# Kernel tuning notes

Measured on AMD Instinct MI355X. Metric: run time of the kernel, lower is better.

The kernel has to match this reference:

```python
import jax, jax.numpy as jnp
import numpy as np

B, LQ, LD = 64, 20, 512
D, NB, WIN = 300, 11, 5
EQ, ED, DESC, KC = 5, 10, 20, 10
VW, VE, VC = 50000, 10000, 5000

# KNRM kernel centers / widths (requires_grad=False buffers in the original)
MU = jnp.array([1.0, 0.9, 0.7, 0.5, 0.3, 0.1, -0.1, -0.3, -0.5, -0.7, -0.9], jnp.float32)
SIGMA = jnp.array([1e-3] + [0.1] * 10, jnp.float32)


def setup_inputs() -> dict:
    key = jax.random.key(0)
    ks = jax.random.split(key, 20)
    f = lambda k, s, sc: jax.random.normal(k, s, jnp.float32) * sc
    return {
        "inputs_qwt": jax.random.randint(ks[0], (B, LQ), 0, VW),
        "inputs_qwm": jnp.ones((B, LQ), jnp.float32),
        "inputs_qei": jax.random.randint(ks[1], (B, EQ), 0, VE),
        "inputs_qet": jax.random.randint(ks[2], (B, EQ * DESC), 0, VW),
        "inputs_qew": jax.random.randint(ks[3], (B, EQ * KC), 0, VC),
        "inputs_qem": jnp.ones((B, EQ), jnp.float32),
        "inputs_dwt": jax.random.randint(ks[4], (B, LD), 0, VW),
        "inputs_dwm": jnp.ones((B, LD), jnp.float32),
        "inputs_dei": jax.random.randint(ks[5], (B, ED), 0, VE),
        "inputs_det": jax.random.randint(ks[6], (B, ED * DESC), 0, VW),
        "inputs_dew": jax.random.randint(ks[7], (B, ED * KC), 0, VC),
        "inputs_dem": jnp.ones((B, ED), jnp.float32),
        "wrd_emb": f(ks[8], (VW, D), 0.1),
        "ent_emb": f(ks[9], (VE, 128), 0.1),
        "car_emb": f(ks[10], (VC, 128), 0.1),
        "bow_W": f(ks[11], (128, D), 0.05), "bow_b": jnp.zeros((128,), jnp.float32),
        "conv_uni_W": f(ks[12], (128, 1, D), 0.05), "conv_uni_b": jnp.zeros((128,), jnp.float32),
        "conv_bi_W": f(ks[13], (128, 2, D), 0.04), "conv_bi_b": jnp.zeros((128,), jnp.float32),
        "conv_tri_W": f(ks[14], (128, 3, D), 0.03), "conv_tri_b": jnp.zeros((128,), jnp.float32),
        "conv_des_W": f(ks[15], (128, WIN, D), 0.02), "conv_des_b": jnp.zeros((128,), jnp.float32),
        "dense_f_W": f(ks[16], (1, 16 * NB), 0.1), "dense_f_b": jnp.zeros((1,), jnp.float32),
    }


def _conv_words(x, w, b):
    # x: [N, L, D]; w: [O, k, D] -> relu conv over the word axis, valid padding -> [N, L-k+1, O]
    k, L = w.shape[1], x.shape[1]
    segs = jnp.stack([x[:, i:L - k + 1 + i] for i in range(k)], axis=2)  # [N, L-k+1, k, D]
    return jax.nn.relu(jnp.einsum('nlkd,okd->nlo', segs, w) + b)


def _l2(x):
    return x / jnp.maximum(jnp.linalg.norm(x, axis=-1, keepdims=True), 1e-10)


def _kernel_pool(q, d, mq, md):
    # q:[B,Lq,128] d:[B,Ld,128] mq:[B,Lq] md:[B,Ld] -> [B, NB]
    sim = jnp.einsum('bqe,bde->bqd', q, d)
    pv = jnp.exp(-0.5 * (sim[..., None] - MU) ** 2 / (SIGMA ** 2)) * md[:, None, :, None]
    lps = jnp.log(jnp.maximum(pv.sum(2), 1e-10)) * 0.01 * mq[:, :, None]
    return lps.sum(1)


def _forward(inputs_qwt, inputs_qwm, inputs_qei, inputs_qet, inputs_qew, inputs_qem,
             inputs_dwt, inputs_dwm, inputs_dei, inputs_det, inputs_dew, inputs_dem,
             wrd_emb, ent_emb, car_emb, bow_W, bow_b,
             conv_uni_W, conv_uni_b, conv_bi_W, conv_bi_b, conv_tri_W, conv_tri_b,
             conv_des_W, conv_des_b, dense_f_W, dense_f_b):
    b = inputs_qwt.shape[0]
    qw = wrd_emb[inputs_qwt]  # [B, LQ, D]
    dw = wrd_emb[inputs_dwt]  # [B, LD, D]

    def ent_branch(ids_e, ids_desc, ids_car, n_ent, w_bow):
        desc = wrd_emb[ids_desc].reshape(b * n_ent, DESC, D)
        e_conv = _conv_words(desc, conv_des_W, conv_des_b).max(1).reshape(b, n_ent, 128)
        t = car_emb[ids_car].reshape(b, n_ent * KC, 128)
        att = jax.nn.softmax((w_bow * t).sum(2).reshape(b, n_ent, KC, 1), axis=2)
        ew = (att * t.reshape(b, n_ent, KC, 128)).sum(2)
        return ent_emb[ids_e] + e_conv + ew

    qw_bow = (jnp.einsum('bld,od->blo', qw, bow_W) + bow_b).sum(1, keepdims=True)  # [B,1,128]
    dw_bow = (jnp.einsum('bld,od->blo', dw, bow_W) + bow_b).sum(1, keepdims=True)
    qs = _l2(ent_branch(inputs_qei, inputs_qet, inputs_qew, EQ, qw_bow))  # [B,5,128]
    ds = _l2(ent_branch(inputs_dei, inputs_det, inputs_dew, ED, dw_bow))  # [B,10,128]

    qu = _l2(_conv_words(qw, conv_uni_W, conv_uni_b))
    qb = _l2(_conv_words(qw, conv_bi_W, conv_bi_b))
    qt = _l2(_conv_words(qw, conv_tri_W, conv_tri_b))
    du = _l2(_conv_words(dw, conv_uni_W, conv_uni_b))
    db = _l2(_conv_words(dw, conv_bi_W, conv_bi_b))
    dt = _l2(_conv_words(dw, conv_tri_W, conv_tri_b))

    mqu, mqb, mqt = inputs_qwm, inputs_qwm[:, :-1], inputs_qwm[:, :-2]
    mdu, mdb, mdt = inputs_dwm, inputs_dwm[:, :-1], inputs_dwm[:, :-2]

    kp = _kernel_pool
    pools = [kp(qu, du, mqu, mdu), kp(qu, dt, mqu, mdt), kp(qu, db, mqu, mdb),
             kp(qb, du, mqb, mdu), kp(qt, du, mqt, mdu), kp(qb, db, mqb, mdb),
             kp(qb, dt, mqb, mdt), kp(qt, db, mqt, mdb), kp(qt, dt, mqt, mdt),
             kp(qs, du, inputs_qem, mdu), kp(qs, db, inputs_qem, mdb), kp(qs, dt, inputs_qem, mdt),
             kp(qu, ds, mqu, inputs_dem), kp(qb, ds, mqb, inputs_dem), kp(qt, ds, mqt, inputs_dem),
             kp(qs, ds, inputs_qem, inputs_dem)]
    feats = jnp.concatenate(pools, axis=1)  # [B, 16*NB]
    return jnp.tanh(feats @ dense_f_W.T + dense_f_b)[:, 0]


def reference(inputs_qwt, inputs_qwm, inputs_qei, inputs_qet, inputs_qew, inputs_qem,
              inputs_dwt, inputs_dwm, inputs_dei, inputs_det, inputs_dew, inputs_dem,
              wrd_emb, ent_emb, car_emb, bow_W, bow_b,
              conv_uni_W, conv_uni_b, conv_bi_W, conv_bi_b, conv_tri_W, conv_tri_b,
              conv_des_W, conv_des_b, dense_f_W, dense_f_b):
    return _forward(inputs_qwt, inputs_qwm, inputs_qei, inputs_qet, inputs_qew, inputs_qem,
                    inputs_dwt, inputs_dwm, inputs_dei, inputs_det, inputs_dew, inputs_dem,
                    wrd_emb, ent_emb, car_emb, bow_W, bow_b,
                    conv_uni_W, conv_uni_b, conv_bi_W, conv_bi_b, conv_tri_W, conv_tri_b,
                    conv_des_W, conv_des_b, dense_f_W, dense_f_b)
```

## Files before the change

kernel.cpp:

```cpp
#include <hip/hip_runtime.h>

typedef unsigned short u16;
typedef unsigned int u32;
typedef __attribute__((ext_vector_type(8))) short bf16x8;
typedef __attribute__((ext_vector_type(4))) float f32x4;

#define DEVI __device__ __forceinline__

namespace {
constexpr int LQ_ = 20, LD_ = 512, D_ = 300;
constexpr int EQ_ = 5, ED_ = 10, KC_ = 10;
constexpr int QROWS = 62, DROWS = 1543;
constexpr int QSTR = 64, DSTR = 1600;
constexpr float MU_H[11] = {1.0f,0.9f,0.7f,0.5f,0.3f,0.1f,-0.1f,-0.3f,-0.5f,-0.7f,-0.9f};
}

__constant__ int P2QT_C[16] = {0,0,0,1,2,1,1,2,2,3,3,3,0,1,2,3};
__constant__ int P2DT_C[16] = {0,2,1,0,0,1,2,1,2,0,1,2,3,3,3,3};
__constant__ int NP_C[4]   = {2,2,4,4};
__constant__ int PPL_C[16] = {0,1,0,0, 2,3,0,0, 2,3,4,5, 4,5,6,7};
__constant__ int SETL_C[16]= {0,0,0,0, 0,0,0,0, 1,1,0,0, 1,1,0,0};

DEVI u16 f2bf(float f){ union{float f;u32 u;} v; v.f=f; u32 r=(v.u+0x7fffu+((v.u>>16)&1u))>>16; return (u16)r; }
DEVI float bf2f(u16 h){ union{u32 u;float f;} v; v.u=((u32)h)<<16; return v.f; }

__global__ __launch_bounds__(256) void k_wpack(const float* __restrict__ Wu, const float* __restrict__ Wb,
                                               const float* __restrict__ Wt, const float* __restrict__ Wd,
                                               u16* __restrict__ Wp){
  const int ts = blockIdx.x/10, ks = blockIdx.x%10;
  const float* W; int kk, tap;
  if(ts==0){W=Wu;kk=1;tap=0;}
  else if(ts<3){W=Wb;kk=2;tap=ts-1;}
  else if(ts<6){W=Wt;kk=3;tap=ts-3;}
  else {W=Wd;kk=5;tap=ts-6;}
  for(int idx=threadIdx.x; idx<4096; idx+=256){
    int n0=idx>>9, lane=(idx>>3)&63, j=idx&7;
    int col=lane&15, kg=lane>>4;
    int d=ks*32+kg*8+j, o=n0*16+col;
    float v = (d<300)? W[((long)o*kk + tap)*300 + d] : 0.f;
    Wp[(((long)(ts*8+n0)*10+ks)*64 + lane)*8 + j] = f2bf(v);
  }
}

__global__ __launch_bounds__(512) void k_main(
    const int* __restrict__ dwt, const int* __restrict__ qwt,
    const int* __restrict__ qet, const int* __restrict__ det,
    const float* __restrict__ emb, const u16* __restrict__ Wp,
    const float* __restrict__ bu, const float* __restrict__ bb, const float* __restrict__ bt,
    const float* __restrict__ bd,
    u16* __restrict__ dcat, u16* __restrict__ qcat,
    float* __restrict__ qdm, float* __restrict__ ddm, float* __restrict__ parts)
{
  __shared__ __align__(16) char smem[77088];
  __shared__ int tokid[80];
  const int bx = blockIdx.x, t = threadIdx.x;
  const int lane=t&63, wave=t>>6, col16=lane&15, kg=lane>>4;
  if(bx < 576){
    const bool isdoc = bx < 512;
    const int seq   = isdoc? (bx>>3) : (bx-512);
    const int l0    = isdoc? (bx&7)*64 : 0;
    const int Ltok  = isdoc? LD_ : LQ_;
    u16* outp = isdoc? dcat : qcat;
    const long seqstride = isdoc? (long)DSTR*128 : (long)QSTR*128;
    u16* xs = (u16*)smem;
    float* ot = (float*)(smem + 43296);
    const int nrows = min(66, Ltok - l0);
    if(t<66) tokid[t] = (t<nrows)? (isdoc? dwt[seq*LD_+l0+t] : qwt[seq*LQ_+t]) : 0;
    __syncthreads();
    for(int idx=t; idx<66*80; idx+=512){
      int r=idx/80, q=idx-r*80;
      ushort4 o4;
      if(q<75 && r<nrows){
        float4 v = ((const float4*)(emb + (long)tokid[r]*D_))[q];
        o4.x=f2bf(v.x); o4.y=f2bf(v.y); o4.z=f2bf(v.z); o4.w=f2bf(v.w);
      } else { o4.x=0;o4.y=0;o4.z=0;o4.w=0; }
      *(ushort4*)&xs[r*328 + q*4] = o4;
    }
    __syncthreads();
    #pragma unroll
    for(int c=0;c<3;c++){
      const int tb = (c==0)?0:((c==1)?1:3);
      const int base = (c==0)?0:((c==1)?Ltok:2*Ltok-1);
      const float* bias = (c==0)?bu:((c==1)?bb:bt);
      f32x4 acc4[4];
      #pragma unroll
      for(int mt=0;mt<4;mt++) acc4[mt]=(f32x4){0.f,0.f,0.f,0.f};
      #pragma unroll
      for(int h=0;h<2;h++){
        bf16x8 wf[15];
        #pragma unroll
        for(int i=0;i<=c;i++)
          #pragma unroll
          for(int k5=0;k5<5;k5++)
            wf[i*5+k5] = *(const bf16x8*)(Wp + (((long)((tb+i)*8 + wave)*10) + h*5 + k5)*512 + lane*8);
        #pragma unroll
        for(int mt=0;mt<4;mt++){
          #pragma unroll
          for(int i=0;i<=c;i++){
            const u16* xrow = &xs[(mt*16 + col16 + i)*328 + h*160 + kg*8];
            #pragma unroll
            for(int k5=0;k5<5;k5++){
              bf16x8 a = *(const bf16x8*)(xrow + k5*32);
              acc4[mt]=__builtin_amdgcn_mfma_f32_16x16x32_bf16(a,wf[i*5+k5],acc4[mt],0,0,0);
            }
          }
        }
      }
      const float bv = bias[wave*16+col16];
      #pragma unroll
      for(int mt=0;mt<4;mt++)
        #pragma unroll
        for(int reg=0;reg<4;reg++)
          ot[(mt*16+kg*4+reg)*132 + wave*16+col16] = fmaxf(acc4[mt][reg]+bv, 0.f);
      __syncthreads();
      {
        const int p = t>>3, j = t&7;
        const int nv = min(64, (Ltok - c) - l0);
        float ss=0.f;
        if(p<nv){
          #pragma unroll
          for(int k=0;k<16;k++){ float v = ot[p*132 + j + 8*k]; ss += v*v; }
        }
        ss += __shfl_xor(ss,1); ss += __shfl_xor(ss,2); ss += __shfl_xor(ss,4);
        if(p<nv){
          float inv = 1.0f/fmaxf(sqrtf(ss),1e-10f);
          u16* ob = outp + (long)seq*seqstride + ((long)(base + l0 + p))*128 + j*16;
          #pragma unroll
          for(int hh=0;hh<2;hh++){
            bf16x8 o8;
            #pragma unroll
            for(int e=0;e<8;e++) o8[e] = (short)f2bf(ot[p*132 + j*16 + hh*8 + e]*inv);
            *(bf16x8*)(ob + hh*8) = o8;
          }
        }
      }
      __syncthreads();
    }
  } else if(bx < 816){
    const int d = bx - 576;
    const bool isq = d < 80;
    const int s0 = (isq? d : d-80)*4;
    const int* dt_ = isq? qet : det;
    float* dm = isq? qdm : ddm;
    u16* xs4 = (u16*)smem;
    if(t<80) tokid[t] = dt_[s0*20 + t];
    __syncthreads();
    for(int idx=t; idx<80*80; idx+=512){
      int lr=idx/80, q=idx-lr*80;
      ushort4 o4;
      if(q<75){
        float4 v = ((const float4*)(emb + (long)tokid[lr]*D_))[q];
        o4.x=f2bf(v.x); o4.y=f2bf(v.y); o4.z=f2bf(v.z); o4.w=f2bf(v.w);
      } else { o4.x=0;o4.y=0;o4.z=0;o4.w=0; }
      *(ushort4*)&xs4[lr*328 + q*4] = o4;
    }
    __syncthreads();
    f32x4 acc4[4];
    #pragma unroll
    for(int s=0;s<4;s++) acc4[s]=(f32x4){0.f,0.f,0.f,0.f};
    #pragma unroll
    for(int h=0;h<2;h++){
      bf16x8 wf[25];
      #pragma unroll
      for(int tap=0;tap<5;tap++)
        #pragma unroll
        for(int k5=0;k5<5;k5++)
          wf[tap*5+k5] = *(const bf16x8*)(Wp + (((long)((6+tap)*8 + wave)*10) + h*5 + k5)*512 + lane*8);
      #pragma unroll
      for(int s=0;s<4;s++){
        #pragma unroll
        for(int tap=0;tap<5;tap++){
          const u16* xrow = &xs4[(s*20 + col16 + tap)*328 + h*160 + kg*8];
          #pragma unroll
          for(int k5=0;k5<5;k5++){
            bf16x8 a = *(const bf16x8*)(xrow + k5*32);
            acc4[s]=__builtin_amdgcn_mfma_f32_16x16x32_bf16(a,wf[tap*5+k5],acc4[s],0,0,0);
          }
        }
      }
    }
    const float bv = bd[wave*16+col16];
    #pragma unroll
    for(int s=0;s<4;s++){
      float m=-1e30f;
      #pragma unroll
      for(int reg=0;reg<4;reg++) m=fmaxf(m, acc4[s][reg]+bv);
      m=fmaxf(m,__shfl_xor(m,16));
      m=fmaxf(m,__shfl_xor(m,32));
      m=fmaxf(m,0.f);
      if(kg==0) dm[(long)(s0+s)*128 + wave*16+col16]=m;
    }
  } else {
    const int idx = bx - 816;
    const int side = idx>>6, b = idx&63;
    const int q = t%80, g = t/80;
    if(g<6){
      float a0=0.f,a1=0.f,a2=0.f,a3=0.f;
      const int L = side? LD_ : LQ_;
      if(q<75){
        for(int r=g; r<L; r+=6){
          const int tok = side? dwt[b*LD_+r] : qwt[b*LQ_+r];
          float4 v = ((const float4*)(emb + (long)tok*D_))[q];
          a0+=v.x; a1+=v.y; a2+=v.z; a3+=v.w;
        }
      }
      if(q<76){
        float4 o4={a0,a1,a2,a3};
        *(float4*)(parts + (((long)side*64 + b)*8 + g)*304 + q*4) = o4;
      }
    }
  }
}

__global__ __launch_bounds__(256) void k_entpost(
    const int* __restrict__ qei, const int* __restrict__ qew,
    const int* __restrict__ dei, const int* __restrict__ dew,
    const float* __restrict__ qdm, const float* __restrict__ ddm,
    const float* __restrict__ parts, const float* __restrict__ bowW, const float* __restrict__ bowb,
    const float* __restrict__ ent, const float* __restrict__ car,
    u16* __restrict__ qcat, u16* __restrict__ dcat)
{
  const int e15 = blockIdx.x, b = blockIdx.y, t = threadIdx.x;
  const bool isq = (e15 < EQ_);
  const int e = isq? e15 : e15-EQ_;
  const float* dmx = isq? (qdm + (long)(b*EQ_+e)*128) : (ddm + (long)(b*ED_+e)*128);
  const int eid = isq? qei[b*EQ_+e] : dei[b*ED_+e];
  const int* carids = isq? (qew + b*EQ_*KC_ + e*KC_) : (dew + b*ED_*KC_ + e*KC_);
  u16* orow = isq? (qcat + ((long)b*QSTR + 57 + e)*128) : (dcat + ((long)b*DSTR + 1533 + e)*128);

  __shared__ float carS[KC_*128];
  __shared__ float sv[304];
  __shared__ float bwS[128];
  __shared__ float sc[KC_], att[KC_];
  __shared__ float red[4];
  const float* p = parts + (((long)(isq?0:1)*64 + b)*8)*304;
  for(int d=t; d<304; d+=256){
    float s=0.f;
    #pragma unroll
    for(int g=0;g<6;g++) s += p[g*304+d];
    sv[d]=s;
  }
  for(int idx=t; idx<KC_*128; idx+=256){
    int j = idx>>7, c = idx&127;
    carS[j*128+c] = car[(long)carids[j]*128 + c];
  }
  __syncthreads();
  {
    const int ch = t>>1, h = t&1;
    float acc=0.f;
    const float* w = bowW + (long)ch*300 + h*150;
    const float* x = sv + h*150;
    for(int d=0; d<150; d++) acc += x[d]*w[d];
    acc += __shfl_xor(acc,1);
    if(h==0) bwS[ch] = acc + (isq? (float)LQ_ : (float)LD_)*bowb[ch];
  }
  __syncthreads();
  {
    const int j = t>>4, l16 = t&15;
    if(j < KC_){
      float s=0.f;
      for(int c=l16;c<128;c+=16) s += bwS[c]*carS[j*128+c];
      s += __shfl_xor(s,1); s += __shfl_xor(s,2); s += __shfl_xor(s,4); s += __shfl_xor(s,8);
      if(l16==0) sc[j]=s;
    }
  }
  __syncthreads();
  if(t==0){
    float m=-1e30f;
    for(int x=0;x<KC_;x++) m = fmaxf(m, sc[x]);
    float ssum=0.f;
    for(int x=0;x<KC_;x++){ float e2=__expf(sc[x]-m); att[x]=e2; ssum+=e2; }
    float rs = 1.0f/ssum;
    for(int x=0;x<KC_;x++) att[x]*=rs;
  }
  __syncthreads();
  float val=0.f;
  if(t<128){
    float ew=0.f;
    for(int x=0;x<KC_;x++) ew += att[x]*carS[x*128+t];
    val = ent[(long)eid*128+t] + dmx[t] + ew;
  }
  float ss = val*val;
  ss += __shfl_xor(ss,1); ss += __shfl_xor(ss,2); ss += __shfl_xor(ss,4);
  ss += __shfl_xor(ss,8); ss += __shfl_xor(ss,16); ss += __shfl_xor(ss,32);
  if((t&63)==0) red[t>>6]=ss;
  __syncthreads();
  if(t<128){
    float nv = 1.0f/fmaxf(sqrtf(red[0]+red[1]),1e-10f);
    orow[t] = f2bf(val*nv);
  }
}

__global__ __launch_bounds__(512) void k_simgauss(const u16* __restrict__ qcat, const u16* __restrict__ dcat,
                                                  const float* __restrict__ dwm, const float* __restrict__ dem,
                                                  float* __restrict__ Spart){
  const int b=blockIdx.x, piece=blockIdx.y;
  const int t=threadIdx.x, lane=t&63, wave=t>>6;
  const int qtile=wave>>1, dpar=wave&1;
  const int col16=lane&15, kg=lane>>4;
  constexpr int NT[4]={8,8,8,1};
  constexpr int TBASE[4]={0,8,16,24};
  constexpr int PEND[4]={512,1023,1533,1543};
  bf16x8 afr[4];
  #pragma unroll
  for(int ks=0;ks<4;ks++)
    afr[ks] = *(const bf16x8*)&qcat[((long)b*QSTR + qtile*16+col16)*128 + ks*32 + kg*8];
  float aP[4][11], aS[4][11];
  #pragma unroll
  for(int r=0;r<4;r++)
    #pragma unroll
    for(int m=0;m<11;m++){ aP[r][m]=0.f; aS[r][m]=0.f; }
  const int t0 = dpar*4;
  const int t1 = (NT[piece] < t0+4)? NT[piece] : t0+4;
  for(int tt=t0; tt<t1; tt++){
    const int tb = TBASE[piece]+tt;
    f32x4 acc[4];
    #pragma unroll
    for(int n0=0;n0<4;n0++) acc[n0]=(f32x4){0.f,0.f,0.f,0.f};
    #pragma unroll
    for(int ks=0;ks<4;ks++){
      #pragma unroll
      for(int n0=0;n0<4;n0++){
        bf16x8 bfr = *(const bf16x8*)&dcat[((long)b*DSTR + tb*64 + n0*16+col16)*128 + ks*32 + kg*8];
        acc[n0]=__builtin_amdgcn_mfma_f32_16x16x32_bf16(afr[ks],bfr,acc[n0],0,0,0);
      }
    }
    #pragma unroll
    for(int n0=0;n0<4;n0++){
      const int col = tb*64 + n0*16 + col16;
      float md;
      if(col<512) md = dwm[b*LD_+col];
      else if(col<1023) md = dwm[b*LD_+col-512];
      else if(col<1533) md = dwm[b*LD_+col-1023];
      else if(col<1543) md = dem[b*ED_+(col-1533)];
      else md = 0.f;
      const bool pr = col < PEND[piece];
      const float mdP = pr? md : 0.f;
      const float mdS = pr? 0.f : md;
      #pragma unroll
      for(int reg=0;reg<4;reg++){
        const float svv = acc[n0][reg];
        {
          float d1 = svv-1.0f;
          float e = __expf(-500000.0f*d1*d1);
          aP[reg][0] += mdP*e; aS[reg][0] += mdS*e;
        }
        #pragma unroll
        for(int m=1;m<11;m++){
          float dm = svv-MU_H[m];
          float e = __expf(-50.0f*dm*dm);
          aP[reg][m] += mdP*e; aS[reg][m] += mdS*e;
        }
      }
    }
  }
  #pragma unroll
  for(int reg=0;reg<4;reg++)
    #pragma unroll
    for(int m=0;m<11;m++){
      float vP=aP[reg][m];
      vP+=__shfl_xor(vP,1); vP+=__shfl_xor(vP,2); vP+=__shfl_xor(vP,4); vP+=__shfl_xor(vP,8);
      aP[reg][m]=vP;
      float vS=aS[reg][m];
      vS+=__shfl_xor(vS,1); vS+=__shfl_xor(vS,2); vS+=__shfl_xor(vS,4); vS+=__shfl_xor(vS,8);
      aS[reg][m]=vS;
    }
  if(col16==0){
    #pragma unroll
    for(int reg=0;reg<4;reg++){
      const int qr = qtile*16 + kg*4 + reg;
      float* o = Spart + (((long)b*64 + qr)*8 + piece*2+dpar)*22;
      #pragma unroll
      for(int m=0;m<11;m++){ o[m]=aP[reg][m]; o[11+m]=aS[reg][m]; }
    }
  }
}

__global__ __launch_bounds__(256) void k_feats(const float* __restrict__ Spart, const float* __restrict__ qwm,
                                               const float* __restrict__ qem, const float* __restrict__ dfW,
                                               const float* __restrict__ dfb, float* __restrict__ out){
  const int b = blockIdx.x, t = threadIdx.x;
  __shared__ float fsh[176];
  __shared__ float red[4];
  if(t<176){
    const int pool = t/11, m = t - pool*11;
    const int qt = P2QT_C[pool], dt = P2DT_C[pool];
    const int qlo = (qt==0)?0:((qt==1)?20:((qt==2)?39:57));
    const int qn  = (qt==0)?20:((qt==1)?19:((qt==2)?18:5));
    float f = 0.f;
    for(int r=0;r<qn;r++){
      const int qr = qlo + r;
      float mq = (qt<3)? qwm[b*LQ_+r] : qem[b*EQ_+r];
      const float* row = Spart + (((long)b*64 + qr)*8)*22 + m;
      float sv = 0.f;
      const int np = NP_C[dt];
      for(int k=0;k<np;k++){
        const int ii = dt*4+k;
        sv += row[PPL_C[ii]*22 + SETL_C[ii]*11];
      }
      f += logf(fmaxf(sv,1e-10f))*0.01f*mq;
    }
    fsh[t] = f;
  }
  __syncthreads();
  float v = (t<176)? fsh[t]*dfW[t] : 0.f;
  v += __shfl_xor(v,1); v += __shfl_xor(v,2); v += __shfl_xor(v,4);
  v += __shfl_xor(v,8); v += __shfl_xor(v,16); v += __shfl_xor(v,32);
  if((t&63)==0) red[t>>6]=v;
  __syncthreads();
  if(t==0) out[b] = tanhf(red[0]+red[1]+red[2]+red[3] + dfb[0]);
}

extern "C" void kernel_launch(void* const* d_in, const int* in_sizes, int n_in,
                              void* d_out, int out_size, void* d_ws, size_t ws_size,
                              hipStream_t stream)
{
  const int*   qwt=(const int*)d_in[0];
  const float* qwm=(const float*)d_in[1];
  const int*   qei=(const int*)d_in[2];
  const int*   qet=(const int*)d_in[3];
  const int*   qew=(const int*)d_in[4];
  const float* qem=(const float*)d_in[5];
  const int*   dwt=(const int*)d_in[6];
  const float* dwm=(const float*)d_in[7];
  const int*   dei=(const int*)d_in[8];
  const int*   det=(const int*)d_in[9];
  const int*   dew=(const int*)d_in[10];
  const float* dem=(const float*)d_in[11];
  const float* emb=(const float*)d_in[12];
  const float* ent=(const float*)d_in[13];
  const float* car=(const float*)d_in[14];
  const float* bowW=(const float*)d_in[15];
  const float* bowb=(const float*)d_in[16];
  const float* Wu=(const float*)d_in[17];
  const float* bu=(const float*)d_in[18];
  const float* Wb=(const float*)d_in[19];
  const float* bb=(const float*)d_in[20];
  const float* Wt=(const float*)d_in[21];
  const float* bt=(const float*)d_in[22];
  const float* Wd=(const float*)d_in[23];
  const float* bd=(const float*)d_in[24];
  const float* dfW=(const float*)d_in[25];
  const float* dfb=(const float*)d_in[26];
  float* out=(float*)d_out;

  char* ws=(char*)d_ws;
  size_t off=0;
  auto A=[&](size_t n){ size_t r=off; off=(off+n+255)&~(size_t)255; return r; };
  u16* Wp     = (u16*)(ws + A((size_t)11*8*10*64*8*2));
  u16* dcat   = (u16*)(ws + A((size_t)64*DSTR*128*2));
  u16* qcat   = (u16*)(ws + A((size_t)64*QSTR*128*2));
  float* qdm  = (float*)(ws + A((size_t)320*128*4));
  float* ddm  = (float*)(ws + A((size_t)640*128*4));
  float* parts= (float*)(ws + A((size_t)2*64*8*304*4));
  float* Spart= (float*)(ws + A((size_t)64*64*8*22*4));
  if(off > ws_size) return;

  k_wpack<<<110,256,0,stream>>>(Wu,Wb,Wt,Wd,Wp);
  k_main<<<944,512,0,stream>>>(dwt,qwt,qet,det,emb,Wp,bu,bb,bt,bd,dcat,qcat,qdm,ddm,parts);
  k_entpost<<<dim3(15,64),256,0,stream>>>(qei,qew,dei,dew,qdm,ddm,parts,bowW,bowb,ent,car,qcat,dcat);
  k_simgauss<<<dim3(64,4),512,0,stream>>>(qcat,dcat,dwm,dem,Spart);
  k_feats<<<64,256,0,stream>>>(Spart,qwm,qem,dfW,dfb,out);
}
```

Measured before the change: 179.6 us.

## Pre-convert embedding table to bf16 and fuse bag-of-words sums into main kernel

A new prep kernel converts the whole fp32 word-embedding table to bf16 on every call, alongside the weight packing. The main kernel's row gathers then read half-width bf16 rows. The separate bag-of-words gather blocks are removed: per-tile sums are now taken from the bf16 rows already staged in shared memory. A small new kernel does the bow projection instead of k_entpost. This targets the duplicated fp32 row gathers, but converting the full 50000-row table each call adds a large streaming pass, and the bow sums now accumulate bf16-rounded values.

```diff
diff --git a/kernel.cpp b/kernel.cpp
--- a/kernel.cpp
+++ b/kernel.cpp
@@ -12,6 +12,7 @@
 constexpr int EQ_ = 5, ED_ = 10, KC_ = 10;
 constexpr int QROWS = 62, DROWS = 1543;
 constexpr int QSTR = 64, DSTR = 1600;
+constexpr int NCVT = 14649;
 constexpr float MU_H[11] = {1.0f,0.9f,0.7f,0.5f,0.3f,0.1f,-0.1f,-0.3f,-0.5f,-0.7f,-0.9f};
 }
 
@@ -24,28 +25,40 @@
 DEVI u16 f2bf(float f){ union{float f;u32 u;} v; v.f=f; u32 r=(v.u+0x7fffu+((v.u>>16)&1u))>>16; return (u16)r; }
 DEVI float bf2f(u16 h){ union{u32 u;float f;} v; v.u=((u32)h)<<16; return v.f; }
 
-__global__ __launch_bounds__(256) void k_wpack(const float* __restrict__ Wu, const float* __restrict__ Wb,
-                                               const float* __restrict__ Wt, const float* __restrict__ Wd,
-                                               u16* __restrict__ Wp){
-  const int ts = blockIdx.x/10, ks = blockIdx.x%10;
-  const float* W; int kk, tap;
-  if(ts==0){W=Wu;kk=1;tap=0;}
-  else if(ts<3){W=Wb;kk=2;tap=ts-1;}
-  else if(ts<6){W=Wt;kk=3;tap=ts-3;}
-  else {W=Wd;kk=5;tap=ts-6;}
-  for(int idx=threadIdx.x; idx<4096; idx+=256){
-    int n0=idx>>9, lane=(idx>>3)&63, j=idx&7;
-    int col=lane&15, kg=lane>>4;
-    int d=ks*32+kg*8+j, o=n0*16+col;
-    float v = (d<300)? W[((long)o*kk + tap)*300 + d] : 0.f;
-    Wp[(((long)(ts*8+n0)*10+ks)*64 + lane)*8 + j] = f2bf(v);
+__global__ __launch_bounds__(256) void k_prep(const float* __restrict__ emb, u16* __restrict__ emb16,
+                                              const float* __restrict__ Wu, const float* __restrict__ Wb,
+                                              const float* __restrict__ Wt, const float* __restrict__ Wd,
+                                              u16* __restrict__ Wp){
+  const int bx = blockIdx.x;
+  if(bx < NCVT){
+    long i4 = (long)bx*256 + threadIdx.x;
+    if(i4 < 3750000){
+      float4 v = ((const float4*)emb)[i4];
+      ushort4 o4; o4.x=f2bf(v.x); o4.y=f2bf(v.y); o4.z=f2bf(v.z); o4.w=f2bf(v.w);
+      ((ushort4*)emb16)[i4] = o4;
+    }
+  } else {
+    const int b2 = bx - NCVT;
+    const int ts = b2/10, ks = b2%10;
+    const float* W; int kk, tap;
+    if(ts==0){W=Wu;kk=1;tap=0;}
+    else if(ts<3){W=Wb;kk=2;tap=ts-1;}
+    else if(ts<6){W=Wt;kk=3;tap=ts-3;}
+    else {W=Wd;kk=5;tap=ts-6;}
+    for(int idx=threadIdx.x; idx<4096; idx+=256){
+      int n0=idx>>9, lane=(idx>>3)&63, j=idx&7;
+      int col=lane&15, kg=lane>>4;
+      int d=ks*32+kg*8+j, o=n0*16+col;
+      float v = (d<300)? W[((long)o*kk + tap)*300 + d] : 0.f;
+      Wp[(((long)(ts*8+n0)*10+ks)*64 + lane)*8 + j] = f2bf(v);
+    }
   }
 }
 
 __global__ __launch_bounds__(512) void k_main(
     const int* __restrict__ dwt, const int* __restrict__ qwt,
     const int* __restrict__ qet, const int* __restrict__ det,
-    const float* __restrict__ emb, const u16* __restrict__ Wp,
+    const u16* __restrict__ emb16, const u16* __restrict__ Wp,
     const float* __restrict__ bu, const float* __restrict__ bb, const float* __restrict__ bt,
     const float* __restrict__ bd,
     u16* __restrict__ dcat, u16* __restrict__ qcat,
@@ -67,14 +80,16 @@
     const int nrows = min(66, Ltok - l0);
     if(t<66) tokid[t] = (t<nrows)? (isdoc? dwt[seq*LD_+l0+t] : qwt[seq*LQ_+t]) : 0;
     __syncthreads();
-    for(int idx=t; idx<66*80; idx+=512){
-      int r=idx/80, q=idx-r*80;
-      ushort4 o4;
-      if(q<75 && r<nrows){
-        float4 v = ((const float4*)(emb + (long)tokid[r]*D_))[q];
-        o4.x=f2bf(v.x); o4.y=f2bf(v.y); o4.z=f2bf(v.z); o4.w=f2bf(v.w);
-      } else { o4.x=0;o4.y=0;o4.z=0;o4.w=0; }
-      *(ushort4*)&xs[r*328 + q*4] = o4;
+    #pragma unroll
+    for(int it=0; it<11; it++){
+      int idx = t + it*512;
+      if(idx < 66*80){
+        int r=idx/80, q=idx-r*80;
+        ushort4 o4;
+        if(q<75 && r<nrows) o4 = *(const ushort4*)(emb16 + (long)tokid[r]*300 + q*4);
+        else { o4.x=0;o4.y=0;o4.z=0;o4.w=0; }
+        *(ushort4*)&xs[r*328 + q*4] = o4;
+      }
     }
     __syncthreads();
     #pragma unroll
@@ -136,7 +151,19 @@
       }
       __syncthreads();
     }
-  } else if(bx < 816){
+    {
+      const int nr = isdoc? 64 : 20;
+      const int g  = isdoc? (bx&7) : 0;
+      const int b  = seq;
+      if(t<304){
+        float s=0.f;
+        if(t<300){
+          for(int r=0;r<nr;r++) s += bf2f(xs[r*328 + t]);
+        }
+        parts[(((long)(isdoc?64:0) + b)*8 + g)*304 + t] = s;
+      }
+    }
+  } else {
     const int d = bx - 576;
     const bool isq = d < 80;
     const int s0 = (isq? d : d-80)*4;
@@ -145,14 +172,16 @@
     u16* xs4 = (u16*)smem;
     if(t<80) tokid[t] = dt_[s0*20 + t];
     __syncthreads();
-    for(int idx=t; idx<80*80; idx+=512){
-      int lr=idx/80, q=idx-lr*80;
-      ushort4 o4;
-      if(q<75){
-        float4 v = ((const float4*)(emb + (long)tokid[lr]*D_))[q];
-        o4.x=f2bf(v.x); o4.y=f2bf(v.y); o4.z=f2bf(v.z); o4.w=f2bf(v.w);
-      } else { o4.x=0;o4.y=0;o4.z=0;o4.w=0; }
-      *(ushort4*)&xs4[lr*328 + q*4] = o4;
+    #pragma unroll
+    for(int it=0; it<13; it++){
+      int idx = t + it*512;
+      if(idx < 80*80){
+        int lr=idx/80, q=idx-lr*80;
+        ushort4 o4;
+        if(q<75) o4 = *(const ushort4*)(emb16 + (long)tokid[lr]*300 + q*4);
+        else { o4.x=0;o4.y=0;o4.z=0;o4.w=0; }
+        *(ushort4*)&xs4[lr*328 + q*4] = o4;
+      }
     }
     __syncthreads();
     f32x4 acc4[4];
@@ -190,33 +219,34 @@
       m=fmaxf(m,0.f);
       if(kg==0) dm[(long)(s0+s)*128 + wave*16+col16]=m;
     }
-  } else {
-    const int idx = bx - 816;
-    const int side = idx>>6, b = idx&63;
-    const int q = t%80, g = t/80;
-    if(g<6){
-      float a0=0.f,a1=0.f,a2=0.f,a3=0.f;
-      const int L = side? LD_ : LQ_;
-      if(q<75){
-        for(int r=g; r<L; r+=6){
-          const int tok = side? dwt[b*LD_+r] : qwt[b*LQ_+r];
-          float4 v = ((const float4*)(emb + (long)tok*D_))[q];
-          a0+=v.x; a1+=v.y; a2+=v.z; a3+=v.w;
-        }
-      }
-      if(q<76){
-        float4 o4={a0,a1,a2,a3};
-        *(float4*)(parts + (((long)side*64 + b)*8 + g)*304 + q*4) = o4;
-      }
-    }
-  }
+  }
+}
+
+__global__ __launch_bounds__(128) void k_bowmat(const float* __restrict__ parts,
+                                                const float* __restrict__ bowW, const float* __restrict__ bowb,
+                                                float* __restrict__ qbow, float* __restrict__ dbow){
+  const int side = blockIdx.x>>6, b = blockIdx.x&63, t = threadIdx.x;
+  __shared__ float sv[304];
+  const float* p = parts + (((long)side*64 + b)*8)*304;
+  const int ng = side? 8 : 1;
+  for(int d=t; d<304; d+=128){
+    float s=0.f;
+    for(int g=0;g<ng;g++) s += p[g*304+d];
+    sv[d]=s;
+  }
+  __syncthreads();
+  float acc=0.f;
+  const float* w = bowW + (long)t*D_;
+  for(int d=0; d<D_; d++) acc += sv[d]*w[d];
+  const float L = side? (float)LD_ : (float)LQ_;
+  (side? dbow:qbow)[b*128+t] = acc + L*bowb[t];
 }
 
 __global__ __launch_bounds__(256) void k_entpost(
     const int* __restrict__ qei, const int* __restrict__ qew,
     const int* __restrict__ dei, const int* __restrict__ dew,
     const float* __restrict__ qdm, const float* __restrict__ ddm,
-    const float* __restrict__ parts, const float* __restrict__ bowW, const float* __restrict__ bowb,
+    const float* __restrict__ qbow, const float* __restrict__ dbow,
     const float* __restrict__ ent, const float* __restrict__ car,
     u16* __restrict__ qcat, u16* __restrict__ dcat)
 {
@@ -224,42 +254,24 @@
   const bool isq = (e15 < EQ_);
   const int e = isq? e15 : e15-EQ_;
   const float* dmx = isq? (qdm + (long)(b*EQ_+e)*128) : (ddm + (long)(b*ED_+e)*128);
+  const float* bw = isq? (qbow + b*128) : (dbow + b*128);
   const int eid = isq? qei[b*EQ_+e] : dei[b*ED_+e];
   const int* carids = isq? (qew + b*EQ_*KC_ + e*KC_) : (dew + b*ED_*KC_ + e*KC_);
   u16* orow = isq? (qcat + ((long)b*QSTR + 57 + e)*128) : (dcat + ((long)b*DSTR + 1533 + e)*128);
 
   __shared__ float carS[KC_*128];
-  __shared__ float sv[304];
-  __shared__ float bwS[128];
   __shared__ float sc[KC_], att[KC_];
   __shared__ float red[4];
-  const float* p = parts + (((long)(isq?0:1)*64 + b)*8)*304;
-  for(int d=t; d<304; d+=256){
-    float s=0.f;
-    #pragma unroll
-    for(int g=0;g<6;g++) s += p[g*304+d];
-    sv[d]=s;
-  }
   for(int idx=t; idx<KC_*128; idx+=256){
     int j = idx>>7, c = idx&127;
     carS[j*128+c] = car[(long)carids[j]*128 + c];
-  }
-  __syncthreads();
-  {
-    const int ch = t>>1, h = t&1;
-    float acc=0.f;
-    const float* w = bowW + (long)ch*300 + h*150;
-    const float* x = sv + h*150;
-    for(int d=0; d<150; d++) acc += x[d]*w[d];
-    acc += __shfl_xor(acc,1);
-    if(h==0) bwS[ch] = acc + (isq? (float)LQ_ : (float)LD_)*bowb[ch];
   }
   __syncthreads();
   {
     const int j = t>>4, l16 = t&15;
     if(j < KC_){
       float s=0.f;
-      for(int c=l16;c<128;c+=16) s += bwS[c]*carS[j*128+c];
+      for(int c=l16;c<128;c+=16) s += bw[c]*carS[j*128+c];
       s += __shfl_xor(s,1); s += __shfl_xor(s,2); s += __shfl_xor(s,4); s += __shfl_xor(s,8);
       if(l16==0) sc[j]=s;
     }
@@ -453,12 +465,16 @@
   float* qdm  = (float*)(ws + A((size_t)320*128*4));
   float* ddm  = (float*)(ws + A((size_t)640*128*4));
   float* parts= (float*)(ws + A((size_t)2*64*8*304*4));
+  float* qbow = (float*)(ws + A((size_t)64*128*4));
+  float* dbow = (float*)(ws + A((size_t)64*128*4));
   float* Spart= (float*)(ws + A((size_t)64*64*8*22*4));
+  u16* emb16  = (u16*)(ws + A((size_t)50000*300*2));
   if(off > ws_size) return;
 
-  k_wpack<<<110,256,0,stream>>>(Wu,Wb,Wt,Wd,Wp);
-  k_main<<<944,512,0,stream>>>(dwt,qwt,qet,det,emb,Wp,bu,bb,bt,bd,dcat,qcat,qdm,ddm,parts);
-  k_entpost<<<dim3(15,64),256,0,stream>>>(qei,qew,dei,dew,qdm,ddm,parts,bowW,bowb,ent,car,qcat,dcat);
+  k_prep<<<NCVT+110,256,0,stream>>>(emb,emb16,Wu,Wb,Wt,Wd,Wp);
+  k_main<<<816,512,0,stream>>>(dwt,qwt,qet,det,emb16,Wp,bu,bb,bt,bd,dcat,qcat,qdm,ddm,parts);
+  k_bowmat<<<128,128,0,stream>>>(parts,bowW,bowb,qbow,dbow);
+  k_entpost<<<dim3(15,64),256,0,stream>>>(qei,qew,dei,dew,qdm,ddm,qbow,dbow,ent,car,qcat,dcat);
   k_simgauss<<<dim3(64,4),512,0,stream>>>(qcat,dcat,dwm,dem,Spart);
   k_feats<<<64,256,0,stream>>>(Spart,qwm,qem,dfW,dfb,out);
 }
```

After: 155.0 us (median of 3 runs). 1.16x faster.
